# Optimization experiments

Hardware: AMD Instinct MI355X
Metric: run time of the kernel (lower is better)

## Reference

```python
import jax, jax.numpy as jnp
import numpy as np


def setup_inputs() -> dict:
    key = jax.random.key(0)
    ks = jax.random.split(key, 8)
    b, n, K, d, MC = 32, 64, 512, 256, 2
    # soft codebook assignments per slot (bounded convex weights)
    encodings = jax.nn.softmax(jax.random.normal(ks[0], (b, n, K), jnp.float32), axis=-1)
    # hypersphere-initialized means (unit-norm rows)
    mu = jax.random.normal(ks[1], (K, d), jnp.float32)
    mu_embeddings = mu / jnp.linalg.norm(mu, axis=-1, keepdims=True)
    sigma_embeddings = jax.random.uniform(ks[2], (K, d), jnp.float32)
    fc1_w = jax.random.normal(ks[3], (K, d, d), jnp.float32) * (1.0 / np.sqrt(d))
    fc1_b = jax.random.normal(ks[4], (K, d), jnp.float32) * 0.02
    fc2_w = jax.random.normal(ks[5], (K, d, d), jnp.float32) * (1.0 / np.sqrt(d))
    fc2_b = jax.random.normal(ks[6], (K, d), jnp.float32) * 0.02
    eps = jax.random.normal(ks[7], (b, MC, n, d), jnp.float32)  # reparam noise
    return {"encodings": encodings, "mu_embeddings": mu_embeddings,
            "sigma_embeddings": sigma_embeddings, "fc1_w": fc1_w, "fc1_b": fc1_b,
            "fc2_w": fc2_w, "fc2_b": fc2_b, "eps": eps}


def reference(encodings, mu_embeddings, sigma_embeddings, fc1_w, fc1_b, fc2_w, fc2_b, eps):
    b, n, K = encodings.shape
    m = eps.shape[1]
    # per-slot Gaussian params from codebook mixture
    slot_mu = jnp.einsum('bnk,kd->bnd', encodings, mu_embeddings)          # (b,n,d)
    slot_sigma = jnp.exp(0.5 * jnp.einsum('bnk,kd->bnd', encodings, sigma_embeddings))
    # reparameterized MC samples: (b,m,n,d)
    slots = slot_mu[:, None] + slot_sigma[:, None] * eps
    # per-token dynamic 2-layer MLP weights (mixture over codebook)
    fc1w = jnp.einsum('bnk,kgh->bngh', encodings, fc1_w)  # (b,n,d,d)
    fc1b = jnp.einsum('bnk,kg->bng', encodings, fc1_b)    # (b,n,d)
    fc2w = jnp.einsum('bnk,kgh->bngh', encodings, fc2_w)
    fc2b = jnp.einsum('bnk,kg->bng', encodings, fc2_b)
    slots = jax.nn.relu(jnp.einsum('bmng,bngh->bmnh', slots, fc1w) + fc1b[:, None])
    slots = jax.nn.relu(jnp.einsum('bmng,bngh->bmnh', slots, fc2w) + fc2b[:, None])
    # rearrange 'b m n d -> (b m) n d'
    return slots.reshape(b * m, n, slots.shape[-1])
```

## Files before the change

### kernel.cpp

```cpp
#include <hip/hip_runtime.h>
#include <hip/hip_bf16.h>

typedef unsigned short u16;
typedef __attribute__((ext_vector_type(8))) short shortx8;
typedef __attribute__((ext_vector_type(4))) float floatx4;

__device__ __forceinline__ float bf2f(u16 u) {
    union { unsigned int ui; float f; } x; x.ui = ((unsigned int)u) << 16; return x.f;
}
__device__ __forceinline__ u16 f2b(float f) {
    union { float f; unsigned int u; } x; x.f = f;
    unsigned int r = (x.u + 0x7fffu + ((x.u >> 16) & 1u)) >> 16;
    return (u16)r;
}
__device__ __forceinline__ void glds16(const void* g, void* l) {
    __builtin_amdgcn_global_load_lds((const __attribute__((address_space(1))) void*)g,
                                     (__attribute__((address_space(3))) void*)l, 16, 0, 0);
}

__global__ __launch_bounds__(256) void cvt_bf16_kernel(const float* __restrict__ src,
                                                       u16* __restrict__ dst, int n) {
    int i = (blockIdx.x * 256 + threadIdx.x) * 4;
    if (i + 3 < n) {
        float4 v = *(const float4*)&src[i];
        ushort4 o; o.x = f2b(v.x); o.y = f2b(v.y); o.z = f2b(v.z); o.w = f2b(v.w);
        *(ushort4*)&dst[i] = o;
    }
}

__global__ __launch_bounds__(256) void build_bsmall_t(const float* __restrict__ mu,
                                                      const float* __restrict__ sg,
                                                      const float* __restrict__ b1,
                                                      const float* __restrict__ b2,
                                                      u16* __restrict__ Bs) {
    __shared__ float t[32][33];
    const float* src;
    int z = blockIdx.z;
    if (z == 0) src = mu; else if (z == 1) src = sg; else if (z == 2) src = b1; else src = b2;
    int k0 = blockIdx.x * 32, c0 = blockIdx.y * 32;
    int r = threadIdx.x >> 3, c4 = (threadIdx.x & 7) * 4;
    float4 v = *(const float4*)&src[(size_t)(k0 + r) * 256 + c0 + c4];
    t[r][c4] = v.x; t[r][c4 + 1] = v.y; t[r][c4 + 2] = v.z; t[r][c4 + 3] = v.w;
    __syncthreads();
    ushort4 o;
    o.x = f2b(t[c4 + 0][r]); o.y = f2b(t[c4 + 1][r]);
    o.z = f2b(t[c4 + 2][r]); o.w = f2b(t[c4 + 3][r]);
    *(ushort4*)&Bs[(size_t)(z * 256 + c0 + r) * 512 + k0 + c4] = o;
}

__global__ __launch_bounds__(256) void cvt_transpose(const float* __restrict__ W,
                                                     u16* __restrict__ Bt) {
    __shared__ float t[32][33];
    int n0 = blockIdx.x * 32, k0 = blockIdx.y * 32;
    int r  = threadIdx.x >> 3, c4 = (threadIdx.x & 7) * 4;
    float4 v = *(const float4*)&W[(size_t)(k0 + r) * 65536 + n0 + c4];
    t[r][c4] = v.x; t[r][c4 + 1] = v.y; t[r][c4 + 2] = v.z; t[r][c4 + 3] = v.w;
    __syncthreads();
    ushort4 o;
    o.x = f2b(t[c4 + 0][r]); o.y = f2b(t[c4 + 1][r]);
    o.z = f2b(t[c4 + 2][r]); o.w = f2b(t[c4 + 3][r]);
    *(ushort4*)&Bt[(size_t)(n0 + r) * 512 + k0 + c4] = o;
}

__global__ __launch_bounds__(256) void slots_kernel(const float* __restrict__ P,
                                                    const float* __restrict__ eps,
                                                    float* __restrict__ slots) {
    int t = blockIdx.x, d = threadIdx.x;
    float mu = P[(size_t)t * 1024 + d];
    float sg = expf(0.5f * P[(size_t)t * 1024 + 256 + d]);
    int b = t >> 6, n = t & 63;
    #pragma unroll
    for (int m = 0; m < 2; m++) {
        float e = eps[(size_t)(((b * 2 + m) * 64) + n) * 256 + d];
        slots[(size_t)t * 512 + m * 256 + d] = mu + sg * e;
    }
}

__global__ __launch_bounds__(256, 2) void gemm_small(const u16* __restrict__ A,
                                                     const u16* __restrict__ B,
                                                     float* __restrict__ C,
                                                     int N, int K,
                                                     int nbx_l2, int bypx_l2) {
    __shared__ __align__(16) u16 As[128 * 64];
    __shared__ __align__(16) u16 Bs[128 * 64];
    int tid = threadIdx.x;
    int wave = tid >> 6, lane = tid & 63;

    int id = blockIdx.x;
    int xcd = id & 7, sq = id >> 3;
    int by = (xcd << bypx_l2) + (sq >> nbx_l2);
    int bx = sq & ((1 << nbx_l2) - 1);
    int m0 = bx * 128, n0 = by * 128;
    int wm = wave >> 1, wn = wave & 1;

    floatx4 acc[4][4];
    #pragma unroll
    for (int r = 0; r < 4; r++)
        #pragma unroll
        for (int c = 0; c < 4; c++)
            #pragma unroll
            for (int q = 0; q < 4; q++) acc[r][c][q] = 0.f;

    int lrsub = lane >> 3, kcl = lane & 7;
    const u16* gA[4]; const u16* gB[4]; u16* lA[4]; u16* lB[4];
    #pragma unroll
    for (int j = 0; j < 4; j++) {
        int r0 = (wave * 4 + j) * 8;
        int row = r0 + lrsub;
        int kof = (kcl ^ (row & 7)) * 8;
        gA[j] = A + (size_t)(m0 + row) * K + kof;
        gB[j] = B + (size_t)(n0 + row) * K + kof;
        lA[j] = As + r0 * 64;
        lB[j] = Bs + r0 * 64;
    }

    int arb = wm * 64 + (lane & 15);
    int brb = wn * 64 + (lane & 15);
    int axr = arb & 7, bxr = brb & 7;
    int cl0 = lane >> 4;

    for (int k0 = 0; k0 < K; k0 += 64) {
        #pragma unroll
        for (int j = 0; j < 4; j++) glds16(gA[j] + k0, lA[j]);
        #pragma unroll
        for (int j = 0; j < 4; j++) glds16(gB[j] + k0, lB[j]);
        __syncthreads();
        #pragma unroll
        for (int s = 0; s < 2; s++) {
            shortx8 af[4], bf[4];
            int ac = ((s * 4 + cl0) ^ axr) * 8;
            int bc = ((s * 4 + cl0) ^ bxr) * 8;
            #pragma unroll
            for (int r = 0; r < 4; r++) af[r] = *(const shortx8*)(As + (arb + r * 16) * 64 + ac);
            #pragma unroll
            for (int c = 0; c < 4; c++) bf[c] = *(const shortx8*)(Bs + (brb + c * 16) * 64 + bc);
            #pragma unroll
            for (int r = 0; r < 4; r++)
                #pragma unroll
                for (int c = 0; c < 4; c++)
                    acc[r][c] = __builtin_amdgcn_mfma_f32_16x16x32_bf16(af[r], bf[c], acc[r][c], 0, 0, 0);
        }
        __syncthreads();
    }

    int crow0 = m0 + wm * 64 + (lane >> 4) * 4;
    int ccol  = n0 + wn * 64 + (lane & 15);
    #pragma unroll
    for (int r = 0; r < 4; r++)
        #pragma unroll
        for (int c = 0; c < 4; c++)
            #pragma unroll
            for (int q = 0; q < 4; q++)
                C[(size_t)(crow0 + r * 16 + q) * N + ccol + c * 16] = acc[r][c][q];
}

__global__ __launch_bounds__(256) void init_y(const float* __restrict__ P,
                                              float* __restrict__ Y, int bias_col) {
    int t = blockIdx.x, h = threadIdx.x;
    float b = P[(size_t)t * 1024 + bias_col + h];
    Y[((size_t)t * 2 + 0) * 256 + h] = b;
    Y[((size_t)t * 2 + 1) * 256 + h] = b;
}

__global__ __launch_bounds__(256, 2) void fused_mlp(const u16* __restrict__ Eb,
                                                    const u16* __restrict__ Bt,
                                                    const float* __restrict__ S,
                                                    float* __restrict__ Y,
                                                    int relu_s) {
    __shared__ __align__(16) u16 As[128 * 64];
    __shared__ __align__(16) u16 Bs[64 * 64];
    __shared__ float sl[16 * 2 * 128];
    int tid = threadIdx.x;
    int wave = tid >> 6, lane = tid & 63;

    int id = blockIdx.x;
    int xcd = id & 7;
    int rest = id >> 3;
    int tt = rest & 15;
    int chi = rest >> 4;
    int combo = chi * 8 + xcd;
    int hh = combo >> 4;
    int gg = combo & 15;
    int m0 = tt * 128;
    int h0 = hh * 64;
    int g0 = gg * 16;

    {
        int g = tid & 15, m = (tid >> 4) & 1, tb = tid >> 5;
        for (int p = 0; p < 16; p++) {
            int t = tb + p * 8;
            float v = S[((size_t)(m0 + t) * 2 + m) * 256 + g0 + g];
            if (relu_s) v = fmaxf(v, 0.f);
            sl[(g * 2 + m) * 128 + t] = v;
        }
    }

    int wm = wave >> 1, wn = wave & 1;
    int lrsub = lane >> 3, kcl = lane & 7;

    const u16* gA[4]; u16* lA[4];
    #pragma unroll
    for (int j = 0; j < 4; j++) {
        int r0 = (wave * 4 + j) * 8;
        int row = r0 + lrsub;
        int kof = (kcl ^ (row & 7)) * 8;
        gA[j] = Eb + (size_t)(m0 + row) * 512 + kof;
        lA[j] = As + r0 * 64;
    }
    const u16* gB[2]; u16* lB[2];
    #pragma unroll
    for (int j = 0; j < 2; j++) {
        int r0 = (wave * 2 + j) * 8;
        int row = r0 + lrsub;
        int kof = (kcl ^ (row & 7)) * 8;
        gB[j] = Bt + ((size_t)g0 * 256 + h0 + row) * 512 + kof;
        lB[j] = Bs + r0 * 64;
    }

    int arb = wm * 64 + (lane & 15);
    int brb = wn * 32 + (lane & 15);
    int axr = arb & 7, bxr = brb & 7;
    int cl0 = lane >> 4;

    floatx4 yreg[2][4][2];
    #pragma unroll
    for (int m = 0; m < 2; m++)
        #pragma unroll
        for (int r = 0; r < 4; r++)
            #pragma unroll
            for (int c = 0; c < 2; c++)
                #pragma unroll
                for (int q = 0; q < 4; q++) yreg[m][r][c][q] = 0.f;

    for (int gi = 0; gi < 16; gi++) {
        size_t gof = (size_t)gi * 256 * 512;
        floatx4 acc[4][2];
        #pragma unroll
        for (int r = 0; r < 4; r++)
            #pragma unroll
            for (int c = 0; c < 2; c++)
                #pragma unroll
                for (int q = 0; q < 4; q++) acc[r][c][q] = 0.f;

        for (int k0 = 0; k0 < 512; k0 += 64) {
            #pragma unroll
            for (int j = 0; j < 4; j++) glds16(gA[j] + k0, lA[j]);
            #pragma unroll
            for (int j = 0; j < 2; j++) glds16(gB[j] + gof + k0, lB[j]);
            __syncthreads();
            #pragma unroll
            for (int s = 0; s < 2; s++) {
                shortx8 af[4], bf[2];
                int ac = ((s * 4 + cl0) ^ axr) * 8;
                int bc = ((s * 4 + cl0) ^ bxr) * 8;
                #pragma unroll
                for (int r = 0; r < 4; r++) af[r] = *(const shortx8*)(As + (arb + r * 16) * 64 + ac);
                #pragma unroll
                for (int c = 0; c < 2; c++) bf[c] = *(const shortx8*)(Bs + (brb + c * 16) * 64 + bc);
                #pragma unroll
                for (int r = 0; r < 4; r++)
                    #pragma unroll
                    for (int c = 0; c < 2; c++)
                        acc[r][c] = __builtin_amdgcn_mfma_f32_16x16x32_bf16(af[r], bf[c], acc[r][c], 0, 0, 0);
            }
            __syncthreads();
        }

        #pragma unroll
        for (int m = 0; m < 2; m++) {
            float4 sq[4];
            #pragma unroll
            for (int r = 0; r < 4; r++)
                sq[r] = *(const float4*)&sl[(gi * 2 + m) * 128 + wm * 64 + cl0 * 4 + r * 16];
            #pragma unroll
            for (int r = 0; r < 4; r++)
                #pragma unroll
                for (int c = 0; c < 2; c++)
                    #pragma unroll
                    for (int q = 0; q < 4; q++)
                        yreg[m][r][c][q] += ((const float*)&sq[r])[q] * acc[r][c][q];
        }
    }

    int l16 = lane & 15;
    #pragma unroll
    for (int m = 0; m < 2; m++)
        #pragma unroll
        for (int r = 0; r < 4; r++)
            #pragma unroll
            for (int c = 0; c < 2; c++)
                #pragma unroll
                for (int q = 0; q < 4; q++) {
                    int t = m0 + wm * 64 + cl0 * 4 + r * 16 + q;
                    int h = h0 + wn * 32 + c * 16 + l16;
                    atomicAdd(&Y[((size_t)t * 2 + m) * 256 + h], yreg[m][r][c][q]);
                }
}

__global__ __launch_bounds__(256) void final_out(const float* __restrict__ Y,
                                                 float* __restrict__ out) {
    int t = blockIdx.x, h = threadIdx.x;
    int b = t >> 6, n = t & 63;
    #pragma unroll
    for (int m = 0; m < 2; m++)
        out[((size_t)((b * 2 + m) * 64) + n) * 256 + h] =
            fmaxf(Y[((size_t)t * 2 + m) * 256 + h], 0.f);
}

extern "C" void kernel_launch(void* const* d_in, const int* in_sizes, int n_in,
                              void* d_out, int out_size, void* d_ws, size_t ws_size,
                              hipStream_t stream) {
    const float* enc = (const float*)d_in[0];
    const float* mu  = (const float*)d_in[1];
    const float* sg  = (const float*)d_in[2];
    const float* f1w = (const float*)d_in[3];
    const float* f1b = (const float*)d_in[4];
    const float* f2w = (const float*)d_in[5];
    const float* f2b = (const float*)d_in[6];
    const float* eps = (const float*)d_in[7];
    float* out = (float*)d_out;

    size_t off = 0;
    auto alloc = [&](size_t b) -> char* {
        char* p = (char*)d_ws + off; off += (b + 255) & ~(size_t)255; return p;
    };
    u16*   Eb    = (u16*)  alloc((size_t)2048 * 512 * 2);
    float* P     = (float*)alloc((size_t)2048 * 1024 * 4);
    float* slots = (float*)alloc((size_t)2048 * 512 * 4);
    float* Y1    = (float*)alloc((size_t)2048 * 512 * 4);
    float* Y2    = (float*)alloc((size_t)2048 * 512 * 4);
    u16*   Bsm   = (u16*)  alloc((size_t)1024 * 512 * 2);
    u16*   Bt    = (u16*)  alloc((size_t)65536 * 512 * 2);

    cvt_bf16_kernel<<<1024, 256, 0, stream>>>(enc, Eb, 2048 * 512);
    build_bsmall_t<<<dim3(16, 8, 4), 256, 0, stream>>>(mu, sg, f1b, f2b, Bsm);
    gemm_small<<<128, 256, 0, stream>>>(Eb, Bsm, P, 1024, 512, 4, 0);
    slots_kernel<<<2048, 256, 0, stream>>>(P, eps, slots);

    cvt_transpose<<<dim3(2048, 16), 256, 0, stream>>>(f1w, Bt);
    init_y<<<2048, 256, 0, stream>>>(P, Y1, 512);
    fused_mlp<<<1024, 256, 0, stream>>>(Eb, Bt, slots, Y1, 0);

    cvt_transpose<<<dim3(2048, 16), 256, 0, stream>>>(f2w, Bt);
    init_y<<<2048, 256, 0, stream>>>(P, Y2, 768);
    fused_mlp<<<1024, 256, 0, stream>>>(Eb, Bt, Y1, Y2, 1);

    final_out<<<2048, 256, 0, stream>>>(Y2, out);
}
```

Measured before the change: 760.2 us.

## Double-buffer LDS tiles to overlap global loads with MFMA compute

Splits the A and B shared-memory tiles into two buffers and prefetches the next k-slice, including the first slice of the next codebook group, while MFMAs run on the current buffer. The per-slice pair of __syncthreads becomes one explicit waitcnt plus barrier. The aim is to hide global-to-LDS latency in the fused MLP GEMM loop. In exchange LDS use doubles, which may reduce occupancy below the two blocks per CU the launch bounds request, and the last iteration issues one wasted wrap-around prefetch.

Measured after the change: 806.4 us. +6.1%, slower.

```diff
diff --git a/kernel.cpp b/kernel.cpp
--- a/kernel.cpp
+++ b/kernel.cpp
@@ -167,8 +167,8 @@
                                                     const float* __restrict__ S,
                                                     float* __restrict__ Y,
                                                     int relu_s) {
-    __shared__ __align__(16) u16 As[128 * 64];
-    __shared__ __align__(16) u16 Bs[64 * 64];
+    __shared__ __align__(16) u16 As[2][128 * 64];
+    __shared__ __align__(16) u16 Bs[2][64 * 64];
     __shared__ float sl[16 * 2 * 128];
     int tid = threadIdx.x;
     int wave = tid >> 6, lane = tid & 63;
@@ -198,23 +198,23 @@
     int wm = wave >> 1, wn = wave & 1;
     int lrsub = lane >> 3, kcl = lane & 7;
 
-    const u16* gA[4]; u16* lA[4];
+    const u16* gA[4]; int lAo[4];
     #pragma unroll
     for (int j = 0; j < 4; j++) {
         int r0 = (wave * 4 + j) * 8;
         int row = r0 + lrsub;
         int kof = (kcl ^ (row & 7)) * 8;
         gA[j] = Eb + (size_t)(m0 + row) * 512 + kof;
-        lA[j] = As + r0 * 64;
-    }
-    const u16* gB[2]; u16* lB[2];
+        lAo[j] = r0 * 64;
+    }
+    const u16* gB[2]; int lBo[2];
     #pragma unroll
     for (int j = 0; j < 2; j++) {
         int r0 = (wave * 2 + j) * 8;
         int row = r0 + lrsub;
         int kof = (kcl ^ (row & 7)) * 8;
         gB[j] = Bt + ((size_t)g0 * 256 + h0 + row) * 512 + kof;
-        lB[j] = Bs + r0 * 64;
+        lBo[j] = r0 * 64;
     }
 
     int arb = wm * 64 + (lane & 15);
@@ -232,8 +232,14 @@
                 #pragma unroll
                 for (int q = 0; q < 4; q++) yreg[m][r][c][q] = 0.f;
 
-    for (int gi = 0; gi < 16; gi++) {
-        size_t gof = (size_t)gi * 256 * 512;
+    #pragma unroll
+    for (int j = 0; j < 4; j++) glds16(gA[j], &As[0][lAo[j]]);
+    #pragma unroll
+    for (int j = 0; j < 2; j++) glds16(gB[j], &Bs[0][lBo[j]]);
+    __syncthreads();
+
+    #pragma unroll 1
+    for (int gi = 0; gi < 16; ++gi) {
         floatx4 acc[4][2];
         #pragma unroll
         for (int r = 0; r < 4; r++)
@@ -242,28 +248,40 @@
                 #pragma unroll
                 for (int q = 0; q < 4; q++) acc[r][c][q] = 0.f;
 
-        for (int k0 = 0; k0 < 512; k0 += 64) {
-            #pragma unroll
-            for (int j = 0; j < 4; j++) glds16(gA[j] + k0, lA[j]);
-            #pragma unroll
-            for (int j = 0; j < 2; j++) glds16(gB[j] + gof + k0, lB[j]);
-            __syncthreads();
+        #pragma unroll
+        for (int kk = 0; kk < 8; ++kk) {
+            const int cb = kk & 1;
+            const int nb = cb ^ 1;
+
+            {
+                const int nkk = (kk + 1) & 7;
+                size_t bgof = (kk < 7)
+                    ? ((size_t)gi * 131072 + (size_t)nkk * 64)
+                    : ((size_t)((gi + 1) & 15) * 131072);
+                #pragma unroll
+                for (int j = 0; j < 4; j++) glds16(gA[j] + nkk * 64, &As[nb][lAo[j]]);
+                #pragma unroll
+                for (int j = 0; j < 2; j++) glds16(gB[j] + bgof, &Bs[nb][lBo[j]]);
+            }
+
             #pragma unroll
             for (int s = 0; s < 2; s++) {
                 shortx8 af[4], bf[2];
                 int ac = ((s * 4 + cl0) ^ axr) * 8;
                 int bc = ((s * 4 + cl0) ^ bxr) * 8;
                 #pragma unroll
-                for (int r = 0; r < 4; r++) af[r] = *(const shortx8*)(As + (arb + r * 16) * 64 + ac);
-                #pragma unroll
-                for (int c = 0; c < 2; c++) bf[c] = *(const shortx8*)(Bs + (brb + c * 16) * 64 + bc);
+                for (int r = 0; r < 4; r++) af[r] = *(const shortx8*)(&As[cb][(arb + r * 16) * 64 + ac]);
+                #pragma unroll
+                for (int c = 0; c < 2; c++) bf[c] = *(const shortx8*)(&Bs[cb][(brb + c * 16) * 64 + bc]);
                 #pragma unroll
                 for (int r = 0; r < 4; r++)
                     #pragma unroll
                     for (int c = 0; c < 2; c++)
                         acc[r][c] = __builtin_amdgcn_mfma_f32_16x16x32_bf16(af[r], bf[c], acc[r][c], 0, 0, 0);
             }
-            __syncthreads();
+
+            asm volatile("s_waitcnt vmcnt(0) lgkmcnt(0)" ::: "memory");
+            __builtin_amdgcn_s_barrier();
         }
 
         #pragma unroll
```

## Process two g-slices per K loop to reuse A tile across both

Applied to the files above, without the earlier changes.

The fused MLP kernel now handles two g indices per pass over K. Each A tile loaded into LDS is reused for two B tiles, which halves A global-to-LDS traffic and the number of barriers per output. The per-thread global pointer arrays are also replaced with single base pointers plus constant offsets, which cuts register use for addressing. In exchange the accumulator count doubles and LDS use grows by one B buffer, which may hurt occupancy under the 2-block launch bound.

Result: faster. 686.0 us (-9.8%).

```diff
diff --git a/kernel.cpp b/kernel.cpp
--- a/kernel.cpp
+++ b/kernel.cpp
@@ -168,7 +168,7 @@
                                                     float* __restrict__ Y,
                                                     int relu_s) {
     __shared__ __align__(16) u16 As[128 * 64];
-    __shared__ __align__(16) u16 Bs[64 * 64];
+    __shared__ __align__(16) u16 Bs[2][64 * 64];
     __shared__ float sl[16 * 2 * 128];
     int tid = threadIdx.x;
     int wave = tid >> 6, lane = tid & 63;
@@ -197,25 +197,13 @@
 
     int wm = wave >> 1, wn = wave & 1;
     int lrsub = lane >> 3, kcl = lane & 7;
-
-    const u16* gA[4]; u16* lA[4];
-    #pragma unroll
-    for (int j = 0; j < 4; j++) {
-        int r0 = (wave * 4 + j) * 8;
-        int row = r0 + lrsub;
-        int kof = (kcl ^ (row & 7)) * 8;
-        gA[j] = Eb + (size_t)(m0 + row) * 512 + kof;
-        lA[j] = As + r0 * 64;
-    }
-    const u16* gB[2]; u16* lB[2];
-    #pragma unroll
-    for (int j = 0; j < 2; j++) {
-        int r0 = (wave * 2 + j) * 8;
-        int row = r0 + lrsub;
-        int kof = (kcl ^ (row & 7)) * 8;
-        gB[j] = Bt + ((size_t)g0 * 256 + h0 + row) * 512 + kof;
-        lB[j] = Bs + r0 * 64;
-    }
+    int kof = (kcl ^ lrsub) * 8;
+
+    const u16* gAb = Eb + (size_t)(m0 + wave * 32 + lrsub) * 512 + kof;
+    const u16* gBb = Bt + ((size_t)g0 * 256 + h0 + wave * 16 + lrsub) * 512 + kof;
+    u16* lAb = As + wave * 2048;
+    u16* lB0 = &Bs[0][wave * 1024];
+    u16* lB1 = &Bs[1][wave * 1024];
 
     int arb = wm * 64 + (lane & 15);
     int brb = wn * 32 + (lane & 15);
@@ -232,53 +220,68 @@
                 #pragma unroll
                 for (int q = 0; q < 4; q++) yreg[m][r][c][q] = 0.f;
 
-    for (int gi = 0; gi < 16; gi++) {
-        size_t gof = (size_t)gi * 256 * 512;
-        floatx4 acc[4][2];
-        #pragma unroll
-        for (int r = 0; r < 4; r++)
-            #pragma unroll
-            for (int c = 0; c < 2; c++)
-                #pragma unroll
-                for (int q = 0; q < 4; q++) acc[r][c][q] = 0.f;
+    #pragma unroll 1
+    for (int gp = 0; gp < 8; gp++) {
+        size_t gof0 = (size_t)(2 * gp) * 131072;
+        size_t gof1 = gof0 + 131072;
+        floatx4 acc[2][4][2];
+        #pragma unroll
+        for (int u = 0; u < 2; u++)
+            #pragma unroll
+            for (int r = 0; r < 4; r++)
+                #pragma unroll
+                for (int c = 0; c < 2; c++)
+                    #pragma unroll
+                    for (int q = 0; q < 4; q++) acc[u][r][c][q] = 0.f;
 
         for (int k0 = 0; k0 < 512; k0 += 64) {
             #pragma unroll
-            for (int j = 0; j < 4; j++) glds16(gA[j] + k0, lA[j]);
-            #pragma unroll
-            for (int j = 0; j < 2; j++) glds16(gB[j] + gof + k0, lB[j]);
+            for (int j = 0; j < 4; j++) glds16(gAb + j * 4096 + k0, lAb + j * 512);
+            #pragma unroll
+            for (int j = 0; j < 2; j++) glds16(gBb + gof0 + j * 4096 + k0, lB0 + j * 512);
+            #pragma unroll
+            for (int j = 0; j < 2; j++) glds16(gBb + gof1 + j * 4096 + k0, lB1 + j * 512);
             __syncthreads();
             #pragma unroll
             for (int s = 0; s < 2; s++) {
-                shortx8 af[4], bf[2];
+                shortx8 af[4], bf[2][2];
                 int ac = ((s * 4 + cl0) ^ axr) * 8;
                 int bc = ((s * 4 + cl0) ^ bxr) * 8;
                 #pragma unroll
                 for (int r = 0; r < 4; r++) af[r] = *(const shortx8*)(As + (arb + r * 16) * 64 + ac);
                 #pragma unroll
-                for (int c = 0; c < 2; c++) bf[c] = *(const shortx8*)(Bs + (brb + c * 16) * 64 + bc);
+                for (int u = 0; u < 2; u++)
+                    #pragma unroll
+                    for (int c = 0; c < 2; c++)
+                        bf[u][c] = *(const shortx8*)(&Bs[u][(brb + c * 16) * 64 + bc]);
+                #pragma unroll
+                for (int r = 0; r < 4; r++)
+                    #pragma unroll
+                    for (int u = 0; u < 2; u++)
+                        #pragma unroll
+                        for (int c = 0; c < 2; c++)
+                            acc[u][r][c] = __builtin_amdgcn_mfma_f32_16x16x32_bf16(af[r], bf[u][c], acc[u][r][c], 0, 0, 0);
+            }
+            __syncthreads();
+        }
+
+        #pragma unroll
+        for (int u = 0; u < 2; u++) {
+            int gi = 2 * gp + u;
+            #pragma unroll
+            for (int m = 0; m < 2; m++) {
+                float4 sq[4];
+                #pragma unroll
+                for (int r = 0; r < 4; r++)
+                    sq[r] = *(const float4*)&sl[(gi * 2 + m) * 128 + wm * 64 + cl0 * 4 + r * 16];
                 #pragma unroll
                 for (int r = 0; r < 4; r++)
                     #pragma unroll
                     for (int c = 0; c < 2; c++)
-                        acc[r][c] = __builtin_amdgcn_mfma_f32_16x16x32_bf16(af[r], bf[c], acc[r][c], 0, 0, 0);
+                        #pragma unroll
+                        for (int q = 0; q < 4; q++)
+                            yreg[m][r][c][q] += ((const float*)&sq[r])[q] * acc[u][r][c][q];
             }
-            __syncthreads();
-        }
-
-        #pragma unroll
-        for (int m = 0; m < 2; m++) {
-            float4 sq[4];
-            #pragma unroll
-            for (int r = 0; r < 4; r++)
-                sq[r] = *(const float4*)&sl[(gi * 2 + m) * 128 + wm * 64 + cl0 * 4 + r * 16];
-            #pragma unroll
-            for (int r = 0; r < 4; r++)
-                #pragma unroll
-                for (int c = 0; c < 2; c++)
-                    #pragma unroll
-                    for (int q = 0; q < 4; q++)
-                        yreg[m][r][c][q] += ((const float*)&sq[r])[q] * acc[r][c][q];
         }
     }
 
```
